# Performance work log

Measured on AMD Instinct MI355X. Metric: run time of the kernel, lower is better.

The kernel has to match this reference:

```python
import jax, jax.numpy as jnp
import numpy as np

B, C, H, W = 8, 128, 64, 64
INTER = C // 2

def setup_inputs() -> dict:
    key = jax.random.key(0)
    ks = jax.random.split(key, 9)
    s = 0.05
    return {
        "x": jax.random.normal(ks[0], (B, C, H, W), dtype=jnp.float32),
        "theta_w": jax.random.normal(ks[1], (INTER, C), dtype=jnp.float32) * s,
        "theta_b": jax.random.normal(ks[2], (INTER,), dtype=jnp.float32) * s,
        "phi_w": jax.random.normal(ks[3], (INTER, C), dtype=jnp.float32) * s,
        "phi_b": jax.random.normal(ks[4], (INTER,), dtype=jnp.float32) * s,
        "g_w": jax.random.normal(ks[5], (INTER, C), dtype=jnp.float32) * s,
        "g_b": jax.random.normal(ks[6], (INTER,), dtype=jnp.float32) * s,
        "out_w": jax.random.normal(ks[7], (C, INTER), dtype=jnp.float32) * s,
        "out_b": jax.random.normal(ks[8], (C,), dtype=jnp.float32) * s,
    }

def reference(x, theta_w, theta_b, phi_w, phi_b, g_w, g_b, out_w, out_b):
    b, c, h, w = x.shape
    xf = x.reshape(b, c, h * w)                                   # [b, C, n]
    # 1x1 convs == per-pixel channel matmuls
    theta = jnp.einsum('oc,bcn->bno', theta_w, xf) + theta_b       # [b, n, inter]
    phi = jnp.einsum('oc,bcn->bon', phi_w, xf) + phi_b[:, None]    # [b, inter, n]
    g = jnp.einsum('oc,bcn->bno', g_w, xf) + g_b                   # [b, n, inter]
    attn = jax.nn.softmax(jnp.einsum('bno,bom->bnm', theta, phi), axis=-1)  # [b, n, n]
    y = jnp.einsum('bnm,bmo->bon', attn, g)                        # [b, inter, n]
    out = jnp.einsum('oc,bcn->bon', out_w, y) + out_b[:, None]     # [b, C, n]
    return out.reshape(b, c, h, w) + x
```

## Files before the change

kernel.cpp:

```cpp
#include <hip/hip_runtime.h>
#include <hip/hip_bf16.h>
#include <cstdint>
#include <cmath>

#define N_PIX 4096
#define CH    128
#define DD    64
#define NBATCH 8
#define NT    32

typedef unsigned short u16;
typedef __attribute__((ext_vector_type(8))) short bf8_t;
typedef __attribute__((ext_vector_type(4))) float f4_t;
typedef __attribute__((ext_vector_type(16))) float f16v;
typedef uint32_t u32x4 __attribute__((ext_vector_type(4)));
typedef uint32_t u32x2 __attribute__((ext_vector_type(2)));

#define L2E 1.44269504088896340736f

#if __has_builtin(__builtin_amdgcn_exp2f)
  #define EXP2(x) __builtin_amdgcn_exp2f(x)
#else
  #define EXP2(x) exp2f(x)
#endif

__device__ __forceinline__ u16 f2b(float f) {
  return __builtin_bit_cast(u16, __float2bfloat16(f));
}
__device__ __forceinline__ float b2f(u16 h) {
  union { uint32_t u; float f; } v; v.u = ((uint32_t)h) << 16;
  return v.f;
}
__device__ __forceinline__ uint32_t pack2(float a, float b) {
  return (uint32_t)f2b(a) | ((uint32_t)f2b(b) << 16);
}
__device__ __forceinline__ float max3f(float a, float b, float c) {
  return fmaxf(fmaxf(a, b), c);
}
__device__ __forceinline__ f4_t mfma16(bf8_t a, bf8_t b, f4_t c) {
  return __builtin_amdgcn_mfma_f32_16x16x32_bf16(a, b, c, 0, 0, 0);
}
__device__ __forceinline__ f16v mfma32(bf8_t a, bf8_t b, f16v c) {
  return __builtin_amdgcn_mfma_f32_32x32x16_bf16(a, b, c, 0, 0, 0);
}
__device__ __forceinline__ void pl32swap(uint32_t &a, uint32_t &b) {
  u32x2 r = __builtin_amdgcn_permlane32_swap(a, b, false, false);
  a = r[0];
  b = r[1];
}

__global__ __launch_bounds__(256) void proj_kernel(
    const float* __restrict__ x,
    const float* __restrict__ tw, const float* __restrict__ tb,
    const float* __restrict__ pw, const float* __restrict__ pb,
    const float* __restrict__ gw, const float* __restrict__ gb,
    u16* __restrict__ theta_h, u16* __restrict__ phi_h, u16* __restrict__ gt_h) {
  __shared__ __align__(16) u16 smem[12800];
  const int blk = blockIdx.x;
  const int b  = blk >> 6;
  const int n0 = (blk & 63) << 6;
  const int tid = threadIdx.x;

  #pragma unroll
  for (int i = 0; i < 8; ++i) {
    int idx = tid + i * 256;
    int px = (idx & 15) * 4;
    int c  = idx >> 4;
    float4 v = *(const float4*)(x + ((size_t)b * CH + c) * N_PIX + n0 + px);
    smem[(px + 0) * 136 + c] = f2b(v.x);
    smem[(px + 1) * 136 + c] = f2b(v.y);
    smem[(px + 2) * 136 + c] = f2b(v.z);
    smem[(px + 3) * 136 + c] = f2b(v.w);
  }
  __syncthreads();

  const int lane = tid & 63;
  const int w    = tid >> 6;
  const int l4   = lane >> 4, l15 = lane & 15;

  bf8_t bw[3][4];
  float bias[3];
  #pragma unroll
  for (int nt = 0; nt < 3; ++nt) {
    int op = 16 * (3 * w + nt) + l15;
    const float* wrow; float bv; float scl;
    if (op < 64)       { wrow = tw + op * CH;          bv = tb[op];        scl = L2E; }
    else if (op < 128) { wrow = pw + (op - 64) * CH;   bv = pb[op - 64];   scl = 1.f; }
    else               { wrow = gw + (op - 128) * CH;  bv = gb[op - 128];  scl = 1.f; }
    bias[nt] = bv * scl;
    #pragma unroll
    for (int ks = 0; ks < 4; ++ks) {
      const float* p = wrow + 32 * ks + l4 * 8;
      bf8_t v;
      #pragma unroll
      for (int j = 0; j < 8; ++j) v[j] = (short)f2b(p[j] * scl);
      bw[nt][ks] = v;
    }
  }

  f4_t acc[4][3];
  #pragma unroll
  for (int mt = 0; mt < 4; ++mt)
    #pragma unroll
    for (int nt = 0; nt < 3; ++nt) acc[mt][nt] = (f4_t){0.f, 0.f, 0.f, 0.f};

  #pragma unroll
  for (int mt = 0; mt < 4; ++mt) {
    #pragma unroll
    for (int ks = 0; ks < 4; ++ks) {
      bf8_t a = *(const bf8_t*)&smem[(l15 + 16 * mt) * 136 + 32 * ks + l4 * 8];
      #pragma unroll
      for (int nt = 0; nt < 3; ++nt)
        acc[mt][nt] = mfma16(a, bw[nt][ks], acc[mt][nt]);
    }
  }
  __syncthreads();

  #pragma unroll
  for (int nt = 0; nt < 3; ++nt) {
    int op = 16 * (3 * w + nt) + l15;
    #pragma unroll
    for (int mt = 0; mt < 4; ++mt) {
      #pragma unroll
      for (int r = 0; r < 4; ++r) {
        int ql = 16 * mt + l4 * 4 + r;
        smem[ql * 200 + op] = f2b(acc[mt][nt][r] + bias[nt]);
      }
    }
  }
  __syncthreads();

  #pragma unroll
  for (int i = 0; i < 4; ++i) {
    int idx = tid + i * 256;
    int q  = idx >> 4;
    int ch = idx & 15;
    uint4 v = *(const uint4*)&smem[q * 200 + ch * 8];
    if (ch < 8)
      *(uint4*)(theta_h + ((size_t)b * N_PIX + n0 + q) * DD + ch * 8) = v;
    else
      *(uint4*)(phi_h + ((size_t)b * N_PIX + n0 + q) * DD + (ch - 8) * 8) = v;
  }
  #pragma unroll
  for (int i = 0; i < 2; ++i) {
    int idx = tid + i * 256;
    int o = idx >> 3;
    int j = idx & 7;
    uint4 v;
    uint32_t* vp = (uint32_t*)&v;
    #pragma unroll
    for (int k = 0; k < 4; ++k) {
      u16 lo = smem[(8 * j + 2 * k) * 200 + 128 + o];
      u16 hi = smem[(8 * j + 2 * k + 1) * 200 + 128 + o];
      vp[k] = (uint32_t)lo | ((uint32_t)hi << 16);
    }
    *(uint4*)(gt_h + ((size_t)b * DD + o) * N_PIX + n0 + 8 * j) = v;
  }
}

__global__ __launch_bounds__(512, 4) void attn_kernel(
    const u16* __restrict__ theta_h, const u16* __restrict__ phi_h,
    const u16* __restrict__ gt_h,
    const float* __restrict__ ow, const float* __restrict__ ob,
    const float* __restrict__ x, float* __restrict__ out) {
  __shared__ __align__(16) u16 smem[32768];

  const int bid = blockIdx.x;
  const int lb  = (bid & 7) * 64 + (bid >> 3);
  const int b   = lb >> 6;
  const int q0  = (lb & 63) << 6;
  const int tid = threadIdx.x;
  const int l   = tid & 63;
  const int w   = tid >> 6;
  const int qg  = w & 1;
  const int mh  = w >> 1;
  const int l31 = l & 31;
  const int hi  = l >> 5;

  bf8_t th[4];
  {
    const u16* trow = theta_h + ((size_t)b * N_PIX + q0 + 32 * qg + l31) * DD;
    #pragma unroll
    for (int kk = 0; kk < 4; ++kk)
      th[kk] = *(const bf8_t*)(trow + 16 * kk + 8 * hi);
  }

  const bf8_t onesA = __builtin_bit_cast(bf8_t,
      (u32x4){0x3F803F80u, 0x3F803F80u, 0x3F803F80u, 0x3F803F80u});

  f16v yacc[2];
  #pragma unroll
  for (int ot = 0; ot < 2; ++ot)
    #pragma unroll
    for (int r = 0; r < 16; ++r) yacc[ot][r] = 0.f;
  f16v y2;
  #pragma unroll
  for (int r = 0; r < 16; ++r) y2[r] = 0.f;
  float m_ = -1e30f;

  const int pr  = tid >> 3, pc = tid & 7;
  const int go  = tid >> 4, gc = tid & 15;
  const u16* phA = phi_h + ((size_t)b * N_PIX + pr) * DD + pc * 8;
  const u16* gtA = gt_h + ((size_t)b * DD + go) * N_PIX + gc * 8;
  const int pO0 = pr * 64 + ((pc ^ (pr & 7)) << 3);
  const int pO1 = pO0 + 4096;
  const int gO0 = 8192 + go * 128 + ((gc ^ (go & 7)) << 3);
  const int gO1 = gO0 + 4096;

  uint4 v0, v1, v2, v3;
  #define LOADS(kb_) do {                                              \
    v0 = *(const uint4*)(phA + (size_t)(kb_) * 8192);                  \
    v1 = *(const uint4*)(phA + (size_t)(kb_) * 8192 + 4096);           \
    v2 = *(const uint4*)(gtA + (size_t)(kb_) * 128);                   \
    v3 = *(const uint4*)(gtA + (size_t)(kb_) * 128 + 32 * (size_t)N_PIX); \
  } while (0)
  #define WRITES(buf_) do {                                            \
    u16* base_ = smem + (buf_) * 16384;                                \
    *(uint4*)(base_ + pO0) = v0;                                       \
    *(uint4*)(base_ + pO1) = v1;                                       \
    *(uint4*)(base_ + gO0) = v2;                                       \
    *(uint4*)(base_ + gO1) = v3;                                       \
  } while (0)

  LOADS(0); WRITES(0);
  __syncthreads();

  const int prow  = 32 * mh + l31;
  const int pbase = prow * 64;
  const int pkey  = prow & 7;

  #pragma unroll 2
  for (int t = 0; t < NT; ++t) {
    const int cur = t & 1;
    if (t < NT - 1) LOADS(t + 1);
    const u16* pb = smem + cur * 16384;
    const u16* gb = pb + 8192;

    f16v st;
    #pragma unroll
    for (int r = 0; r < 16; ++r) st[r] = 0.f;
    __builtin_amdgcn_s_setprio(1);
    #pragma unroll
    for (int kk = 0; kk < 4; ++kk) {
      bf8_t a = *(const bf8_t*)(pb + pbase + (((2 * kk + hi) ^ pkey) << 3));
      st = mfma32(a, th[kk], st);
    }
    __builtin_amdgcn_s_setprio(0);

    float t0 = max3f(st[0],  st[1],  st[2]);
    float t1 = max3f(st[3],  st[4],  st[5]);
    float t2 = max3f(st[6],  st[7],  st[8]);
    float t3 = max3f(st[9],  st[10], st[11]);
    float t4 = max3f(st[12], st[13], st[14]);
    float pmax = fmaxf(max3f(t0, t1, t2), max3f(t3, t4, st[15]));
    pmax = fmaxf(pmax, __shfl_xor(pmax, 32));

    if (!__all(pmax <= m_ + 8.f)) {
      float mn = fmaxf(m_, pmax);
      float sc = EXP2(m_ - mn);
      m_ = mn;
      y2[0] *= sc;
      #pragma unroll
      for (int ot = 0; ot < 2; ++ot)
        #pragma unroll
        for (int r = 0; r < 16; ++r) yacc[ot][r] *= sc;
    }

    #pragma unroll
    for (int r = 0; r < 16; ++r) st[r] = EXP2(st[r] - m_);

    uint32_t c0 = pack2(st[0],  st[1]),  c1 = pack2(st[2],  st[3]);
    uint32_t c2 = pack2(st[4],  st[5]),  c3 = pack2(st[6],  st[7]);
    uint32_t c4 = pack2(st[8],  st[9]),  c5 = pack2(st[10], st[11]);
    uint32_t c6 = pack2(st[12], st[13]), c7 = pack2(st[14], st[15]);
    pl32swap(c0, c2); pl32swap(c1, c3);
    pl32swap(c4, c6); pl32swap(c5, c7);
    bf8_t pf0 = __builtin_bit_cast(bf8_t, (u32x4){c0, c1, c2, c3});
    bf8_t pf1 = __builtin_bit_cast(bf8_t, (u32x4){c4, c5, c6, c7});

    __builtin_amdgcn_s_setprio(1);
    y2 = mfma32(onesA, pf0, y2);
    y2 = mfma32(onesA, pf1, y2);
    #pragma unroll
    for (int ot = 0; ot < 2; ++ot) {
      int orow  = 32 * ot + l31;
      int obase = orow * 128;
      int okey  = orow & 7;
      bf8_t g0 = *(const bf8_t*)(gb + obase + ((((mh << 2) + hi)     ^ okey) << 3));
      yacc[ot] = mfma32(g0, pf0, yacc[ot]);
      bf8_t g1 = *(const bf8_t*)(gb + obase + ((((mh << 2) + 2 + hi) ^ okey) << 3));
      yacc[ot] = mfma32(g1, pf1, yacc[ot]);
    }
    __builtin_amdgcn_s_setprio(0);

    if (t < NT - 1) WRITES(cur ^ 1);
    __syncthreads();
  }
  #undef LOADS
  #undef WRITES

  float l_ = y2[0];

  #pragma unroll
  for (int ot = 0; ot < 2; ++ot)
    #pragma unroll
    for (int r = 0; r < 16; ++r) {
      int o = 32 * ot + (r & 3) + 8 * (r >> 2) + 4 * hi;
      smem[(((qg * 4 + mh) * 64 + o) << 5) + l31] = f2b(yacc[ot][r]);
    }
  float* ml = (float*)(smem + 16384);
  if (hi == 0) {
    ml[(qg * 4 + mh) * 64 + l31]      = m_;
    ml[(qg * 4 + mh) * 64 + 32 + l31] = l_;
  }
  __syncthreads();

  u16* y_lds = smem + 17408;
  {
    const int qg2 = tid >> 8;
    const int rem = tid & 255;
    const int qq  = rem & 31;
    const int og  = rem >> 5;
    float mi[4], li[4];
    #pragma unroll
    for (int i = 0; i < 4; ++i) {
      mi[i] = ml[(qg2 * 4 + i) * 64 + qq];
      li[i] = ml[(qg2 * 4 + i) * 64 + 32 + qq];
    }
    float M = fmaxf(fmaxf(mi[0], mi[1]), fmaxf(mi[2], mi[3]));
    float e[4], L = 0.f;
    #pragma unroll
    for (int i = 0; i < 4; ++i) { e[i] = EXP2(mi[i] - M); L += li[i] * e[i]; }
    float invL = 1.0f / L;
    float acc[8];
    #pragma unroll
    for (int oo = 0; oo < 8; ++oo) {
      int o = og * 8 + oo;
      float a = 0.f;
      #pragma unroll
      for (int i = 0; i < 4; ++i)
        a += b2f(smem[(((qg2 * 4 + i) * 64 + o) << 5) + qq]) * e[i];
      acc[oo] = a * invL;
    }
    uint4 ov;
    ov.x = pack2(acc[0], acc[1]);
    ov.y = pack2(acc[2], acc[3]);
    ov.z = pack2(acc[4], acc[5]);
    ov.w = pack2(acc[6], acc[7]);
    *(uint4*)(y_lds + (32 * qg2 + qq) * 72 + og * 8) = ov;
  }
  __syncthreads();

  {
    const int ct = w & 3;
    const int qt = w >> 2;
    f16v oacc;
    #pragma unroll
    for (int r = 0; r < 16; ++r) oacc[r] = 0.f;
    #pragma unroll
    for (int kk = 0; kk < 4; ++kk) {
      const float* wp = ow + (size_t)(32 * ct + l31) * DD + 16 * kk + 8 * hi;
      bf8_t av;
      #pragma unroll
      for (int j = 0; j < 8; ++j) av[j] = (short)f2b(wp[j]);
      bf8_t bv = *(const bf8_t*)(y_lds + (32 * qt + l31) * 72 + 16 * kk + 8 * hi);
      oacc = mfma32(av, bv, oacc);
    }
    #pragma unroll
    for (int r = 0; r < 16; ++r) {
      int c = 32 * ct + (r & 3) + 8 * (r >> 2) + 4 * hi;
      size_t gi = ((size_t)b * CH + c) * N_PIX + q0 + 32 * qt + l31;
      out[gi] = oacc[r] + ob[c] + x[gi];
    }
  }
}

extern "C" void kernel_launch(void* const* d_in, const int* in_sizes, int n_in,
                              void* d_out, int out_size, void* d_ws, size_t ws_size,
                              hipStream_t stream) {
  const float* x  = (const float*)d_in[0];
  const float* tw = (const float*)d_in[1];
  const float* tb = (const float*)d_in[2];
  const float* pw = (const float*)d_in[3];
  const float* pb = (const float*)d_in[4];
  const float* gw = (const float*)d_in[5];
  const float* gb = (const float*)d_in[6];
  const float* ow = (const float*)d_in[7];
  const float* ob = (const float*)d_in[8];
  float* out = (float*)d_out;

  const size_t sz = (size_t)NBATCH * N_PIX * DD;
  u16* theta_h = (u16*)d_ws;
  u16* phi_h   = theta_h + sz;
  u16* gt_h    = phi_h + sz;

  proj_kernel<<<512, 256, 0, stream>>>(x, tw, tb, pw, pb, gw, gb,
                                       theta_h, phi_h, gt_h);
  attn_kernel<<<512, 512, 0, stream>>>(theta_h, phi_h, gt_h, ow, ob, x, out);
}
```

Measured before the change: 78.76 us.

## Pre-convert projection weights to bf16 and use smaller-tile projection kernel

Adds a small kernel that converts the theta/phi/g weights to bf16 once per call, folding the log2(e) scale into theta, and stores them in workspace. A new projection kernel then loads the weight fragments straight into registers, works on 32-pixel tiles over 1024 blocks with half the shared memory, and computes all 192 outputs with MFMA. The aim is to drop the per-block weight conversion and staging cost and to raise occupancy and parallelism in the projection stage. In exchange it adds one more kernel launch, and it only runs when the workspace is large enough.

Measured after the change: 82.36 us. 1.05x slower.

```diff
diff --git a/kernel.cpp b/kernel.cpp
--- a/kernel.cpp
+++ b/kernel.cpp
@@ -47,6 +47,122 @@
   u32x2 r = __builtin_amdgcn_permlane32_swap(a, b, false, false);
   a = r[0];
   b = r[1];
+}
+
+__global__ __launch_bounds__(256) void wcvt_kernel(
+    const float* __restrict__ tw, const float* __restrict__ pw,
+    const float* __restrict__ gw, u16* __restrict__ wq) {
+  int i = blockIdx.x * 256 + threadIdx.x;
+  float v;
+  if (i < 8192)       v = tw[i] * L2E;
+  else if (i < 16384) v = pw[i - 8192];
+  else                v = gw[i - 16384];
+  wq[i] = f2b(v);
+}
+
+__global__ __launch_bounds__(256) void proj_kernel_q(
+    const float* __restrict__ x,
+    const float* __restrict__ tb, const float* __restrict__ pb,
+    const float* __restrict__ gb, const u16* __restrict__ wq,
+    u16* __restrict__ theta_h, u16* __restrict__ phi_h, u16* __restrict__ gt_h) {
+  __shared__ __align__(16) u16 smem[6400];
+  const int blk = blockIdx.x;
+  const int b  = blk >> 7;
+  const int n0 = (blk & 127) << 5;
+  const int tid = threadIdx.x;
+
+  #pragma unroll
+  for (int i = 0; i < 4; ++i) {
+    int idx = tid + i * 256;
+    int px = (idx & 7) * 4;
+    int c  = idx >> 3;
+    int m  = px >> 2;
+    float4 v = *(const float4*)(x + ((size_t)b * CH + c) * N_PIX + n0 + px);
+    int base = px * 136 + (((c >> 3) ^ m) << 3) + (c & 7);
+    smem[base]       = f2b(v.x);
+    smem[base + 136] = f2b(v.y);
+    smem[base + 272] = f2b(v.z);
+    smem[base + 408] = f2b(v.w);
+  }
+  __syncthreads();
+
+  const int lane = tid & 63;
+  const int w    = tid >> 6;
+  const int l4   = lane >> 4, l15 = lane & 15;
+
+  bf8_t bw[3][4];
+  float bias[3];
+  #pragma unroll
+  for (int nt = 0; nt < 3; ++nt) {
+    int op = 16 * (3 * w + nt) + l15;
+    float bv;
+    if (op < 64)       bv = tb[op] * L2E;
+    else if (op < 128) bv = pb[op - 64];
+    else               bv = gb[op - 128];
+    bias[nt] = bv;
+    #pragma unroll
+    for (int ks = 0; ks < 4; ++ks)
+      bw[nt][ks] = *(const bf8_t*)(wq + (size_t)op * CH + 32 * ks + l4 * 8);
+  }
+
+  f4_t acc[2][3];
+  #pragma unroll
+  for (int mt = 0; mt < 2; ++mt)
+    #pragma unroll
+    for (int nt = 0; nt < 3; ++nt) acc[mt][nt] = (f4_t){0.f, 0.f, 0.f, 0.f};
+
+  #pragma unroll
+  for (int mt = 0; mt < 2; ++mt) {
+    int row = l15 + 16 * mt;
+    #pragma unroll
+    for (int ks = 0; ks < 4; ++ks) {
+      int ch = (4 * ks + l4) ^ (row >> 2);
+      bf8_t a = *(const bf8_t*)&smem[row * 136 + (ch << 3)];
+      #pragma unroll
+      for (int nt = 0; nt < 3; ++nt)
+        acc[mt][nt] = mfma16(a, bw[nt][ks], acc[mt][nt]);
+    }
+  }
+  __syncthreads();
+
+  #pragma unroll
+  for (int nt = 0; nt < 3; ++nt) {
+    int op = 16 * (3 * w + nt) + l15;
+    #pragma unroll
+    for (int mt = 0; mt < 2; ++mt) {
+      #pragma unroll
+      for (int r = 0; r < 4; ++r) {
+        int ql = 16 * mt + l4 * 4 + r;
+        smem[ql * 200 + op] = f2b(acc[mt][nt][r] + bias[nt]);
+      }
+    }
+  }
+  __syncthreads();
+
+  #pragma unroll
+  for (int i = 0; i < 2; ++i) {
+    int idx = tid + i * 256;
+    int q  = idx >> 4;
+    int ch = idx & 15;
+    uint4 v = *(const uint4*)&smem[q * 200 + ch * 8];
+    if (ch < 8)
+      *(uint4*)(theta_h + ((size_t)b * N_PIX + n0 + q) * DD + ch * 8) = v;
+    else
+      *(uint4*)(phi_h + ((size_t)b * N_PIX + n0 + q) * DD + (ch - 8) * 8) = v;
+  }
+  {
+    int o = tid >> 2;
+    int j = tid & 3;
+    uint4 v;
+    uint32_t* vp = (uint32_t*)&v;
+    #pragma unroll
+    for (int k = 0; k < 4; ++k) {
+      u16 lo = smem[(8 * j + 2 * k) * 200 + 128 + o];
+      u16 hi = smem[(8 * j + 2 * k + 1) * 200 + 128 + o];
+      vp[k] = (uint32_t)lo | ((uint32_t)hi << 16);
+    }
+    *(uint4*)(gt_h + ((size_t)b * DD + o) * N_PIX + n0 + 8 * j) = v;
+  }
 }
 
 __global__ __launch_bounds__(256) void proj_kernel(
@@ -393,8 +509,16 @@
   u16* theta_h = (u16*)d_ws;
   u16* phi_h   = theta_h + sz;
   u16* gt_h    = phi_h + sz;
-
-  proj_kernel<<<512, 256, 0, stream>>>(x, tw, tb, pw, pb, gw, gb,
-                                       theta_h, phi_h, gt_h);
+  u16* wq      = gt_h + sz;
+
+  const size_t need = (3 * sz + 24576) * sizeof(u16);
+  if (ws_size >= need) {
+    wcvt_kernel<<<96, 256, 0, stream>>>(tw, pw, gw, wq);
+    proj_kernel_q<<<1024, 256, 0, stream>>>(x, tb, pb, gb, wq,
+                                            theta_h, phi_h, gt_h);
+  } else {
+    proj_kernel<<<512, 256, 0, stream>>>(x, tw, tb, pw, pb, gw, gb,
+                                         theta_h, phi_h, gt_h);
+  }
   attn_kernel<<<512, 512, 0, stream>>>(theta_h, phi_h, gt_h, ow, ob, x, out);
 }
```
